# Optimization experiments

Hardware: AMD Instinct MI355X
Metric: run time of the kernel (lower is better)

The kernel has to match this reference:

```python
import jax, jax.numpy as jnp
import numpy as np

B, S, D = 32, 8192, 256

def setup_inputs() -> dict:
    key = jax.random.key(0)
    k1, k2 = jax.random.split(key)
    sequence = jax.random.normal(k1, (B, S, D), dtype=jnp.float32)
    vector = jax.random.normal(k2, (B, D), dtype=jnp.float32)
    sequence_mask = jnp.ones((B, S), dtype=jnp.float32)
    return {"sequence": sequence, "vector": vector, "sequence_mask": sequence_mask}

def _masked_softmax(logits, mask):
    # stable masked softmax: exp(logits - max) * mask, renormalized
    m = jnp.max(logits, axis=-1, keepdims=True)
    e = jnp.exp(logits - m) * mask
    return e / (jnp.sum(e, axis=-1, keepdims=True) + 1e-13)

def reference(sequence, vector, sequence_mask):
    # DotProduct similarity for every word at once (replaces the per-word loop)
    # scores: [B, S]
    scores = jnp.einsum('bsd,bd->bs', sequence, vector)
    attn = _masked_softmax(scores, sequence_mask)  # [B, S]
    # attention pooling: weighted sum over the sequence -> [B, D]
    pooled = jnp.einsum('bs,bsd->bd', attn, sequence)
    return (pooled, attn)
```

## Files before the change

### kernel.cpp

```cpp
#include <hip/hip_runtime.h>
#include <math.h>

constexpr int NB  = 32;
constexpr int NS  = 8192;
constexpr int ND  = 256;
constexpr int BPB = 64;
constexpr int RPB = NS / BPB;
constexpr int NWAVES = 4;
constexpr int RBATCH = 8;
constexpr int NITER  = RPB / (NWAVES * RBATCH);
constexpr int PSTRIDE = ND + 2;
constexpr int NPART = NWAVES * 2;
constexpr int K2PB = 8;

__global__ __launch_bounds__(256) void k1_partial(
    const float* __restrict__ seq,
    const float* __restrict__ vec,
    const float* __restrict__ mask,
    float* __restrict__ scores,
    float* __restrict__ partials)
{
    const int blk   = blockIdx.x;
    const int b     = blk / BPB;
    const int chunk = blk % BPB;
    const int tid   = threadIdx.x;
    const int lane  = tid & 63;
    const int wave  = tid >> 6;
    const int h     = lane >> 5;
    const int sl    = lane & 31;

    const float* vb = vec + b * ND + sl * 8;
    const float4 v0 = *reinterpret_cast<const float4*>(vb);
    const float4 v1 = *reinterpret_cast<const float4*>(vb + 4);

    float  m = -1e30f;
    float  l = 0.f;
    float4 o0 = make_float4(0.f, 0.f, 0.f, 0.f);
    float4 o1 = make_float4(0.f, 0.f, 0.f, 0.f);

    const int row0 = chunk * RPB;
    const float* __restrict__ seqb   = seq  + (size_t)b * NS * ND;
    const float* __restrict__ maskb  = mask + (size_t)b * NS;
    float* __restrict__       scoreb = scores + (size_t)b * NS;

    const int   sbase = row0 + wave * RBATCH + h * 4;
    const float* base = seqb + (size_t)sbase * ND + sl * 8;

    float4 xa0[4], xa1[4], xb0[4], xb1[4];

    auto LOAD = [&](float4 (&x0)[4], float4 (&x1)[4], int it) {
        const float* p = base + (size_t)it * (NWAVES * RBATCH) * ND;
        #pragma unroll
        for (int k = 0; k < 4; ++k) {
            x0[k] = *reinterpret_cast<const float4*>(p + (size_t)k * ND);
            x1[k] = *reinterpret_cast<const float4*>(p + (size_t)k * ND + 4);
        }
    };

    auto PROC = [&](const float4 (&x0)[4], const float4 (&x1)[4], int it) {
        float dot[4];
        #pragma unroll
        for (int k = 0; k < 4; ++k)
            dot[k] = x0[k].x * v0.x + x0[k].y * v0.y + x0[k].z * v0.z + x0[k].w * v0.w
                   + x1[k].x * v1.x + x1[k].y * v1.y + x1[k].z * v1.z + x1[k].w * v1.w;
        #pragma unroll
        for (int off = 1; off < 32; off <<= 1) {
            #pragma unroll
            for (int k = 0; k < 4; ++k)
                dot[k] += __shfl_xor(dot[k], off, 64);
        }
        const int s0h = sbase + it * (NWAVES * RBATCH);
        if (sl == 0)
            *reinterpret_cast<float4*>(scoreb + s0h) =
                make_float4(dot[0], dot[1], dot[2], dot[3]);
        const float4 mk = *reinterpret_cast<const float4*>(maskb + s0h);

        const float mx = fmaxf(fmaxf(dot[0], dot[1]), fmaxf(dot[2], dot[3]));
        const float mn = fmaxf(m, mx);
        const float scale = __expf(m - mn);
        float e[4];
        e[0] = __expf(dot[0] - mn) * mk.x;
        e[1] = __expf(dot[1] - mn) * mk.y;
        e[2] = __expf(dot[2] - mn) * mk.z;
        e[3] = __expf(dot[3] - mn) * mk.w;
        l    = l    * scale + e[0] + e[1] + e[2] + e[3];
        o0.x = o0.x * scale; o0.y = o0.y * scale; o0.z = o0.z * scale; o0.w = o0.w * scale;
        o1.x = o1.x * scale; o1.y = o1.y * scale; o1.z = o1.z * scale; o1.w = o1.w * scale;
        #pragma unroll
        for (int k = 0; k < 4; ++k) {
            o0.x += e[k] * x0[k].x; o0.y += e[k] * x0[k].y;
            o0.z += e[k] * x0[k].z; o0.w += e[k] * x0[k].w;
            o1.x += e[k] * x1[k].x; o1.y += e[k] * x1[k].y;
            o1.z += e[k] * x1[k].z; o1.w += e[k] * x1[k].w;
        }
        m = mn;
    };

    LOAD(xa0, xa1, 0);
    #pragma unroll
    for (int it = 0; it < NITER; ++it) {
        if ((it & 1) == 0) {
            if (it + 1 < NITER) LOAD(xb0, xb1, it + 1);
            PROC(xa0, xa1, it);
        } else {
            if (it + 1 < NITER) LOAD(xa0, xa1, it + 1);
            PROC(xb0, xb1, it);
        }
    }

    __shared__ float so[NPART][ND];
    __shared__ float sml[NPART][2];
    const int u = wave * 2 + h;
    *reinterpret_cast<float4*>(&so[u][sl * 8])     = o0;
    *reinterpret_cast<float4*>(&so[u][sl * 8 + 4]) = o1;
    if (sl == 0) { sml[u][0] = m; sml[u][1] = l; }
    __syncthreads();

    float M = sml[0][0];
    #pragma unroll
    for (int i = 1; i < NPART; ++i) M = fmaxf(M, sml[i][0]);
    float L = 0.f, O = 0.f;
    #pragma unroll
    for (int i = 0; i < NPART; ++i) {
        const float wgt = __expf(sml[i][0] - M);
        L += sml[i][1] * wgt;
        O += so[i][tid] * wgt;
    }
    float* p = partials + (size_t)blk * PSTRIDE;
    p[tid] = O;
    if (tid == 0) { p[ND] = M; p[ND + 1] = L; }
}

__global__ __launch_bounds__(256) void k2_fused(
    const float* __restrict__ partials,
    const float* __restrict__ mask,
    float* __restrict__ pooled,
    float* __restrict__ attn)
{
    const int b   = blockIdx.x >> 3;
    const int j   = blockIdx.x & (K2PB - 1);
    const int tid = threadIdx.x;
    __shared__ float w[BPB];
    __shared__ float sM, sL;
    const float* __restrict__ pb = partials + (size_t)b * BPB * PSTRIDE;

    if (tid < BPB) {
        const float mi = pb[tid * PSTRIDE + ND];
        float M = mi;
        #pragma unroll
        for (int off = 32; off > 0; off >>= 1)
            M = fmaxf(M, __shfl_xor(M, off, 64));
        const float li = pb[tid * PSTRIDE + ND + 1];
        const float wi = __expf(mi - M);
        w[tid] = wi;
        float L = li * wi;
        #pragma unroll
        for (int off = 32; off > 0; off >>= 1)
            L += __shfl_xor(L, off, 64);
        if (tid == 0) { sM = M; sL = L; }
    }
    __syncthreads();

    const float M  = sM;
    const float rL = 1.0f / (sL + 1e-13f);

    if (j == 0) {
        float acc = 0.f;
        #pragma unroll 8
        for (int i = 0; i < BPB; ++i)
            acc += pb[i * PSTRIDE + tid] * w[i];
        pooled[b * ND + tid] = acc * rL;
    }

    const int s0 = j * (NS / K2PB) + tid * 4;
    float* ap = attn + (size_t)b * NS + s0;
    const float* mp = mask + (size_t)b * NS + s0;
    float4 sc = *reinterpret_cast<float4*>(ap);
    const float4 mk = *reinterpret_cast<const float4*>(mp);
    sc.x = __expf(sc.x - M) * mk.x * rL;
    sc.y = __expf(sc.y - M) * mk.y * rL;
    sc.z = __expf(sc.z - M) * mk.z * rL;
    sc.w = __expf(sc.w - M) * mk.w * rL;
    *reinterpret_cast<float4*>(ap) = sc;
}

extern "C" void kernel_launch(void* const* d_in, const int* in_sizes, int n_in,
                              void* d_out, int out_size, void* d_ws, size_t ws_size,
                              hipStream_t stream)
{
    const float* seq  = (const float*)d_in[0];
    const float* vec  = (const float*)d_in[1];
    const float* mask = (const float*)d_in[2];

    float* pooled = (float*)d_out;
    float* attn   = pooled + NB * ND;

    float* partials = (float*)d_ws;

    k1_partial<<<NB * BPB, 256, 0, stream>>>(seq, vec, mask, attn, partials);
    k2_fused<<<NB * K2PB, 256, 0, stream>>>(partials, mask, pooled, attn);
}
```

Before: 50.49 us.

## Remap lanes to 16-lane row groups with 64 contiguous bytes per lane

Reassigns the wave's work so each 16-lane group owns one row and each lane loads 16 contiguous floats, where before each 32-lane half covered four rows with 8 floats per lane. This cuts the cross-lane shuffle reduction from five steps on four dots to four steps on two dots, and shrinks the per-step softmax bookkeeping. In exchange the block has twice as many partial accumulators to merge in shared memory, mask and score accesses become scalar per row instead of float4, and register use goes up for the larger per-lane vectors.

```diff
diff --git a/kernel.cpp b/kernel.cpp
--- a/kernel.cpp
+++ b/kernel.cpp
@@ -10,7 +10,7 @@
 constexpr int RBATCH = 8;
 constexpr int NITER  = RPB / (NWAVES * RBATCH);
 constexpr int PSTRIDE = ND + 2;
-constexpr int NPART = NWAVES * 2;
+constexpr int NPART = NWAVES * 4;
 constexpr int K2PB = 8;
 
 __global__ __launch_bounds__(256) void k1_partial(
@@ -26,72 +26,72 @@
     const int tid   = threadIdx.x;
     const int lane  = tid & 63;
     const int wave  = tid >> 6;
-    const int h     = lane >> 5;
-    const int sl    = lane & 31;
-
-    const float* vb = vec + b * ND + sl * 8;
-    const float4 v0 = *reinterpret_cast<const float4*>(vb);
-    const float4 v1 = *reinterpret_cast<const float4*>(vb + 4);
+    const int g     = lane >> 4;
+    const int q     = lane & 15;
+
+    const float* vb = vec + b * ND + q * 16;
+    float4 v[4];
+    #pragma unroll
+    for (int j = 0; j < 4; ++j)
+        v[j] = *reinterpret_cast<const float4*>(vb + j * 4);
 
     float  m = -1e30f;
     float  l = 0.f;
-    float4 o0 = make_float4(0.f, 0.f, 0.f, 0.f);
-    float4 o1 = make_float4(0.f, 0.f, 0.f, 0.f);
+    float4 o[4];
+    #pragma unroll
+    for (int j = 0; j < 4; ++j) o[j] = make_float4(0.f, 0.f, 0.f, 0.f);
 
     const int row0 = chunk * RPB;
     const float* __restrict__ seqb   = seq  + (size_t)b * NS * ND;
     const float* __restrict__ maskb  = mask + (size_t)b * NS;
     float* __restrict__       scoreb = scores + (size_t)b * NS;
 
-    const int   sbase = row0 + wave * RBATCH + h * 4;
-    const float* base = seqb + (size_t)sbase * ND + sl * 8;
+    const int    sbase  = row0 + wave * RBATCH;
+    const size_t rowoff = (size_t)g * ND;
+    const float* base   = seqb + (size_t)sbase * ND + q * 16;
 
     float4 xa0[4], xa1[4], xb0[4], xb1[4];
 
     auto LOAD = [&](float4 (&x0)[4], float4 (&x1)[4], int it) {
-        const float* p = base + (size_t)it * (NWAVES * RBATCH) * ND;
-        #pragma unroll
-        for (int k = 0; k < 4; ++k) {
-            x0[k] = *reinterpret_cast<const float4*>(p + (size_t)k * ND);
-            x1[k] = *reinterpret_cast<const float4*>(p + (size_t)k * ND + 4);
+        const float* p = base + (size_t)it * (NWAVES * RBATCH) * ND + rowoff;
+        #pragma unroll
+        for (int j = 0; j < 4; ++j) {
+            x0[j] = *reinterpret_cast<const float4*>(p + j * 4);
+            x1[j] = *reinterpret_cast<const float4*>(p + (size_t)4 * ND + j * 4);
         }
     };
 
     auto PROC = [&](const float4 (&x0)[4], const float4 (&x1)[4], int it) {
-        float dot[4];
-        #pragma unroll
-        for (int k = 0; k < 4; ++k)
-            dot[k] = x0[k].x * v0.x + x0[k].y * v0.y + x0[k].z * v0.z + x0[k].w * v0.w
-                   + x1[k].x * v1.x + x1[k].y * v1.y + x1[k].z * v1.z + x1[k].w * v1.w;
-        #pragma unroll
-        for (int off = 1; off < 32; off <<= 1) {
-            #pragma unroll
-            for (int k = 0; k < 4; ++k)
-                dot[k] += __shfl_xor(dot[k], off, 64);
-        }
-        const int s0h = sbase + it * (NWAVES * RBATCH);
-        if (sl == 0)
-            *reinterpret_cast<float4*>(scoreb + s0h) =
-                make_float4(dot[0], dot[1], dot[2], dot[3]);
-        const float4 mk = *reinterpret_cast<const float4*>(maskb + s0h);
-
-        const float mx = fmaxf(fmaxf(dot[0], dot[1]), fmaxf(dot[2], dot[3]));
-        const float mn = fmaxf(m, mx);
+        float dot0 = 0.f, dot1 = 0.f;
+        #pragma unroll
+        for (int j = 0; j < 4; ++j) {
+            dot0 += x0[j].x * v[j].x + x0[j].y * v[j].y + x0[j].z * v[j].z + x0[j].w * v[j].w;
+            dot1 += x1[j].x * v[j].x + x1[j].y * v[j].y + x1[j].z * v[j].z + x1[j].w * v[j].w;
+        }
+        #pragma unroll
+        for (int off = 1; off < 16; off <<= 1) {
+            dot0 += __shfl_xor(dot0, off, 64);
+            dot1 += __shfl_xor(dot1, off, 64);
+        }
+        const int s = sbase + it * (NWAVES * RBATCH);
+        if (q == 0) {
+            scoreb[s + g]     = dot0;
+            scoreb[s + 4 + g] = dot1;
+        }
+        const float mk0 = maskb[s + g];
+        const float mk1 = maskb[s + 4 + g];
+
+        const float mn    = fmaxf(m, fmaxf(dot0, dot1));
         const float scale = __expf(m - mn);
-        float e[4];
-        e[0] = __expf(dot[0] - mn) * mk.x;
-        e[1] = __expf(dot[1] - mn) * mk.y;
-        e[2] = __expf(dot[2] - mn) * mk.z;
-        e[3] = __expf(dot[3] - mn) * mk.w;
-        l    = l    * scale + e[0] + e[1] + e[2] + e[3];
-        o0.x = o0.x * scale; o0.y = o0.y * scale; o0.z = o0.z * scale; o0.w = o0.w * scale;
-        o1.x = o1.x * scale; o1.y = o1.y * scale; o1.z = o1.z * scale; o1.w = o1.w * scale;
-        #pragma unroll
-        for (int k = 0; k < 4; ++k) {
-            o0.x += e[k] * x0[k].x; o0.y += e[k] * x0[k].y;
-            o0.z += e[k] * x0[k].z; o0.w += e[k] * x0[k].w;
-            o1.x += e[k] * x1[k].x; o1.y += e[k] * x1[k].y;
-            o1.z += e[k] * x1[k].z; o1.w += e[k] * x1[k].w;
+        const float e0 = __expf(dot0 - mn) * mk0;
+        const float e1 = __expf(dot1 - mn) * mk1;
+        l = l * scale + e0 + e1;
+        #pragma unroll
+        for (int j = 0; j < 4; ++j) {
+            o[j].x = o[j].x * scale + e0 * x0[j].x + e1 * x1[j].x;
+            o[j].y = o[j].y * scale + e0 * x0[j].y + e1 * x1[j].y;
+            o[j].z = o[j].z * scale + e0 * x0[j].z + e1 * x1[j].z;
+            o[j].w = o[j].w * scale + e0 * x0[j].w + e1 * x1[j].w;
         }
         m = mn;
     };
@@ -110,10 +110,11 @@
 
     __shared__ float so[NPART][ND];
     __shared__ float sml[NPART][2];
-    const int u = wave * 2 + h;
-    *reinterpret_cast<float4*>(&so[u][sl * 8])     = o0;
-    *reinterpret_cast<float4*>(&so[u][sl * 8 + 4]) = o1;
-    if (sl == 0) { sml[u][0] = m; sml[u][1] = l; }
+    const int u = wave * 4 + g;
+    #pragma unroll
+    for (int j = 0; j < 4; ++j)
+        *reinterpret_cast<float4*>(&so[u][q * 16 + j * 4]) = o[j];
+    if (q == 0) { sml[u][0] = m; sml[u][1] = l; }
     __syncthreads();
 
     float M = sml[0][0];
```

After: 50.87 us. No clear change (+0.7%).
